# Performance work log

Hardware: AMD Instinct MI355X
Metric: run time of the kernel (lower is better)

## Reference

```python
import jax, jax.numpy as jnp
import numpy as np

N_NODES = 100000


def gcn_conv(x, edge_index, edge_weight, W, b, num_nodes):
    """PyG-style GCNConv: add self-loops, symmetric normalization, aggregate, linear."""
    src, dst = edge_index[0], edge_index[1]
    loop = jnp.arange(num_nodes, dtype=src.dtype)
    src_f = jnp.concatenate([src, loop])
    dst_f = jnp.concatenate([dst, loop])
    w_f = jnp.concatenate([edge_weight, jnp.ones((num_nodes,), dtype=edge_weight.dtype)])

    # symmetric normalization D^-1/2 A_hat D^-1/2
    deg = jax.ops.segment_sum(w_f, dst_f, num_segments=num_nodes)
    dinv = jnp.where(deg > 0, jax.lax.rsqrt(deg), 0.0)
    norm = dinv[src_f] * w_f * dinv[dst_f]  # [E + N]

    h = x @ W  # transform first (small out dim) -> cheaper gather/scatter
    msg = h[src_f] * norm[:, None]  # [E + N, out]
    out = jax.ops.segment_sum(msg, dst_f, num_segments=num_nodes)
    return out + b


def setup_inputs() -> dict:
    key = jax.random.key(0)
    k = jax.random.split(key, 7)
    N, E, F, H, C = N_NODES, 3200000, 64, 32, 5
    x = jax.random.normal(k[0], (N, F), dtype=jnp.float32)
    edge_index = jax.random.randint(k[1], (2, E), 0, N, dtype=jnp.int64)
    edge_attr = jax.random.uniform(k[2], (E,), dtype=jnp.float32)
    # Glorot-style init for GCNConv weights, zero bias (PyG default)
    W1 = jax.random.normal(k[3], (F, H), dtype=jnp.float32) * (1.0 / np.sqrt(F))
    b1 = jnp.zeros((H,), dtype=jnp.float32)
    W2 = jax.random.normal(k[4], (H, C), dtype=jnp.float32) * (1.0 / np.sqrt(H))
    b2 = jnp.zeros((C,), dtype=jnp.float32)
    return {"x": x, "edge_index": edge_index, "edge_attr": edge_attr,
            "W1": W1, "b1": b1, "W2": W2, "b2": b2}


def reference(x, edge_index, edge_attr, W1, b1, W2, b2):
    # Dropout is identity in eval mode.
    x1 = gcn_conv(x, edge_index, edge_attr, W1, b1, N_NODES)
    x1 = jax.nn.relu(x1)
    x2 = gcn_conv(x1, edge_index, edge_attr, W2, b2, N_NODES)
    return (x2, x1)
```

## Files before the change

kernel.cpp:

```cpp
#include <hip/hip_runtime.h>

#define NN 100000
#define NE 3200000
#define FIN 64
#define FH 32
#define FO 5
#define NB 1000
#define NPB 100
#define NBIN (4*NPB)
#define QDIV 25000
#define GC 512
#define EPB (NE/GC)
#define KPT 25
#define APAD 6252
#define DPAD 6272
#define CAP 3584
#define WQS 32767.f
#define WQI (1.0f/32767.f)

__device__ __forceinline__ int detect64(const int* __restrict__ ei, int* sflag, int tid) {
    if (tid < 64) {
        int v = ei[2 * tid + 1];
        unsigned long long m = __ballot(v == 0);
        if (tid == 0) *sflag = (m == ~0ULL) ? 1 : 0;
    }
    __syncthreads();
    return *sflag;
}

__device__ __forceinline__ unsigned bf16r(float f) {
    unsigned u = __float_as_uint(f);
    return (u + 0x7FFFu + ((u >> 16) & 1u)) >> 16;
}
__device__ __forceinline__ float blo(unsigned u) { return __uint_as_float(u << 16); }
__device__ __forceinline__ float bhi(unsigned u) { return __uint_as_float(u & 0xFFFF0000u); }

__global__ void k_fillC(const int* __restrict__ ei, const float* __restrict__ w,
                        int* __restrict__ cntRM, int* __restrict__ locRM,
                        unsigned* __restrict__ edata_a, unsigned char* __restrict__ edata_d) {
    __shared__ unsigned stage_a[EPB];
    __shared__ unsigned char stage_d[EPB];
    __shared__ int hist[NB];
    __shared__ int hoff[NB];
    __shared__ int sscan[256];
    __shared__ int sflag;
    int tid = threadIdx.x, g = blockIdx.x;
    for (int i = tid; i < NB; i += 256) hist[i] = 0;
    int is64 = detect64(ei, &sflag, tid);
    __syncthreads();
    int base = g * EPB;
    int myd[KPT];
#pragma unroll
    for (int k = 0; k < KPT; ++k) {
        int e = base + tid + k * 256;
        int dst = -1;
        if (e < base + EPB) {
            dst = is64 ? ei[2 * NE + 2 * e] : ei[NE + e];
            atomicAdd(&hist[dst / NPB], 1);
        }
        myd[k] = dst;
    }
    __syncthreads();
    for (int i = tid; i < NB; i += 256) cntRM[g * NB + i] = hist[i];
    int b0 = tid * 4;
    int c0 = (b0 + 0 < NB) ? hist[b0 + 0] : 0;
    int c1 = (b0 + 1 < NB) ? hist[b0 + 1] : 0;
    int c2 = (b0 + 2 < NB) ? hist[b0 + 2] : 0;
    int c3 = (b0 + 3 < NB) ? hist[b0 + 3] : 0;
    sscan[tid] = c0 + c1 + c2 + c3;
    __syncthreads();
    for (int off = 1; off < 256; off <<= 1) {
        int v = (tid >= off) ? sscan[tid - off] : 0;
        __syncthreads();
        sscan[tid] += v;
        __syncthreads();
    }
    int excl = sscan[tid] - (c0 + c1 + c2 + c3);
    if (b0 + 0 < NB) { hoff[b0 + 0] = excl;                locRM[g * NB + b0 + 0] = excl; }
    if (b0 + 1 < NB) { hoff[b0 + 1] = excl + c0;           locRM[g * NB + b0 + 1] = excl + c0; }
    if (b0 + 2 < NB) { hoff[b0 + 2] = excl + c0 + c1;      locRM[g * NB + b0 + 2] = excl + c0 + c1; }
    if (b0 + 3 < NB) { hoff[b0 + 3] = excl + c0 + c1 + c2; locRM[g * NB + b0 + 3] = excl + c0 + c1 + c2; }
    __syncthreads();
#pragma unroll
    for (int k = 0; k < KPT; ++k) {
        int e = base + tid + k * 256;
        if (e < base + EPB) {
            int src = is64 ? ei[2 * e] : ei[e];
            int dst = myd[k];
            int b = dst / NPB;
            int dloc = dst - b * NPB;
            unsigned wq = (unsigned)(w[e] * WQS + 0.5f);
            int pos = atomicAdd(&hoff[b], 1);
            stage_a[pos] = (unsigned)src | (wq << 17);
            stage_d[pos] = (unsigned char)dloc;
        }
    }
    __syncthreads();
    unsigned* ga = edata_a + (size_t)g * APAD;
    int4* ga4 = (int4*)ga;
    const int NI4 = EPB / 4;
    for (int i = tid; i < NI4; i += 256) {
        int4 v;
        v.x = (int)stage_a[4 * i];     v.y = (int)stage_a[4 * i + 1];
        v.z = (int)stage_a[4 * i + 2]; v.w = (int)stage_a[4 * i + 3];
        ga4[i] = v;
    }
    if (tid < EPB - NI4 * 4) ga[NI4 * 4 + tid] = stage_a[NI4 * 4 + tid];
    unsigned* gd = (unsigned*)(edata_d + (size_t)g * DPAD);
    const int ND = (EPB + 3) / 4;
    for (int i = tid; i < ND; i += 256) {
        unsigned b0v = stage_d[4 * i];
        unsigned b1v = (4 * i + 1 < EPB) ? stage_d[4 * i + 1] : 0;
        unsigned b2v = (4 * i + 2 < EPB) ? stage_d[4 * i + 2] : 0;
        unsigned b3v = (4 * i + 3 < EPB) ? stage_d[4 * i + 3] : 0;
        gd[i] = b0v | (b1v << 8) | (b2v << 16) | (b3v << 24);
    }
}

__global__ __launch_bounds__(512) void k_nodecsr(
        const int* __restrict__ cntRM, const int* __restrict__ locRM,
        const unsigned* __restrict__ edata_a, const unsigned char* __restrict__ edata_d,
        unsigned* __restrict__ edata2,
        int* __restrict__ rowS, int* __restrict__ rowE, float* __restrict__ dinv) {
    __shared__ unsigned s1a[CAP];
    __shared__ unsigned char s1d[CAP];
    __shared__ unsigned s2a[CAP];
    __shared__ int cnt[NBIN];
    __shared__ int loc[NBIN];
    __shared__ int cur[NBIN];
    __shared__ int sc[512];
    __shared__ int sBlen;
    int bi = blockIdx.x, tid = threadIdx.x;
    int b = (bi & 7) * (NB / 8) + (bi >> 3);
    int base = b * CAP;
    int g = tid;
    int len  = cntRM[g * NB + b];
    int lloc = locRM[g * NB + b];
    const unsigned* A = edata_a + (size_t)g * APAD + lloc;
    const unsigned char* D = edata_d + (size_t)g * DPAD + lloc;
    for (int i = tid; i < NBIN; i += 512) cnt[i] = 0;
    sc[tid] = len;
    __syncthreads();
    for (int off = 1; off < 512; off <<= 1) {
        int x = (tid >= off) ? sc[tid - off] : 0;
        __syncthreads();
        sc[tid] += x;
        __syncthreads();
    }
    int sdst = sc[tid] - len;
    if (tid == 511) sBlen = sc[511];
    __syncthreads();
    int blen = sBlen;
    if (blen <= CAP) {
        for (int k = 0; k < len; ++k) {
            unsigned a = A[k];
            int dloc = D[k];
            int src = (int)(a & 0x1FFFF);
            atomicAdd(&cnt[(dloc << 2) | (src / QDIV)], 1);
            s1a[sdst + k] = a;
            s1d[sdst + k] = (unsigned char)dloc;
        }
        __syncthreads();
        int v = (tid < NBIN) ? cnt[tid] : 0;
        sc[tid] = v;
        __syncthreads();
        for (int off = 1; off < 512; off <<= 1) {
            int x = (tid >= off) ? sc[tid - off] : 0;
            __syncthreads();
            sc[tid] += x;
            __syncthreads();
        }
        if (tid < NBIN) { loc[tid] = sc[tid] - v; cur[tid] = sc[tid] - v; }
        __syncthreads();
        if (tid < NPB) {
            rowS[b * NPB + tid] = base + loc[4 * tid];
            rowE[b * NPB + tid] = base + ((tid == NPB - 1) ? blen : loc[4 * tid + 4]);
        }
        for (int j = tid; j < blen; j += 512) {
            unsigned a = s1a[j];
            int dloc = s1d[j];
            int src = (int)(a & 0x1FFFF);
            int pos = atomicAdd(&cur[(dloc << 2) | (src / QDIV)], 1);
            s2a[pos] = a;
        }
        __syncthreads();
        if (tid < NPB) {
            int e0 = loc[4 * tid];
            int e1 = (tid == NPB - 1) ? blen : loc[4 * tid + 4];
            int isum = 0;
            for (int j = e0; j < e1; ++j) isum += (int)(s2a[j] >> 17);
            dinv[b * NPB + tid] = rsqrtf(1.0f + (float)isum * WQI);
        }
        for (int j = tid; j < blen; j += 512) edata2[base + j] = s2a[j];
    } else {
        int* degI = (int*)s1a;
        if (tid < NPB) degI[tid] = 0;
        __syncthreads();
        for (int k = 0; k < len; ++k) {
            unsigned a = A[k];
            int dloc = D[k];
            int src = (int)(a & 0x1FFFF);
            atomicAdd(&cnt[(dloc << 2) | (src / QDIV)], 1);
            atomicAdd(&degI[dloc], (int)(a >> 17));
        }
        __syncthreads();
        int v = (tid < NBIN) ? cnt[tid] : 0;
        sc[tid] = v;
        __syncthreads();
        for (int off = 1; off < 512; off <<= 1) {
            int x = (tid >= off) ? sc[tid - off] : 0;
            __syncthreads();
            sc[tid] += x;
            __syncthreads();
        }
        if (tid < NBIN) { loc[tid] = sc[tid] - v; cur[tid] = base + sc[tid] - v; }
        __syncthreads();
        if (tid < NPB) {
            int e1 = (tid == NPB - 1) ? blen : loc[4 * tid + 4];
            if (e1 > CAP) e1 = CAP;
            int e0 = loc[4 * tid]; if (e0 > CAP) e0 = CAP;
            rowS[b * NPB + tid] = base + e0;
            rowE[b * NPB + tid] = base + e1;
            dinv[b * NPB + tid] = rsqrtf(1.0f + (float)degI[tid] * WQI);
        }
        __syncthreads();
        for (int k = 0; k < len; ++k) {
            unsigned a = A[k];
            int dloc = D[k];
            int src = (int)(a & 0x1FFFF);
            int pos = atomicAdd(&cur[(dloc << 2) | (src / QDIV)], 1);
            if (pos < base + CAP) edata2[pos] = a;
        }
    }
}

__global__ void k_gemm1(const float* __restrict__ x, const float* __restrict__ W1,
                        const float* __restrict__ dinv, unsigned* __restrict__ hs1b) {
    __shared__ float Ws[FIN * FH];
    __shared__ float Xs[16 * FIN];
    int tid = threadIdx.x;
    for (int i = tid; i < FIN * FH; i += 256) Ws[i] = W1[i];
    int row0 = blockIdx.x * 16;
    for (int i = tid; i < 16 * FIN; i += 256) Xs[i] = x[row0 * FIN + i];
    __syncthreads();
    int l = tid & 15, r = tid >> 4;
    int n = row0 + r;
    float a0 = 0.f, a1 = 0.f;
    const float* xr = &Xs[r * FIN];
#pragma unroll
    for (int f = 0; f < FIN; ++f) {
        float xv = xr[f];
        a0 += xv * Ws[f * FH + 2 * l];
        a1 += xv * Ws[f * FH + 2 * l + 1];
    }
    float di = dinv[n];
    hs1b[n * 16 + l] = bf16r(di * a0) | (bf16r(di * a1) << 16);
}

__global__ void k_pull1(const int* __restrict__ rowS, const int* __restrict__ rowE,
                        const unsigned* __restrict__ ed,
                        const unsigned* __restrict__ hs1b, const float* __restrict__ dinv,
                        const float* __restrict__ b1, const float* __restrict__ W2,
                        float* __restrict__ x1out, unsigned* __restrict__ hs2b) {
    __shared__ float Ws2[FH * FO];
    int tid = threadIdx.x;
    if (tid < FH * FO) Ws2[tid] = W2[tid];
    __syncthreads();
    int l = tid & 15;
    int n = blockIdx.x * 16 + (tid >> 4);
    int s = rowS[n], t = rowE[n];
    unsigned su = hs1b[n * 16 + l];
    float a0 = blo(su), a1 = bhi(su);
    int i = s;
    for (; i + 8 <= t; i += 8) {
        unsigned c0 = ed[i],     c1 = ed[i + 1], c2 = ed[i + 2], c3 = ed[i + 3];
        unsigned c4 = ed[i + 4], c5 = ed[i + 5], c6 = ed[i + 6], c7 = ed[i + 7];
        unsigned u0 = hs1b[(c0 & 0x1FFFF) * 16 + l];
        unsigned u1 = hs1b[(c1 & 0x1FFFF) * 16 + l];
        unsigned u2 = hs1b[(c2 & 0x1FFFF) * 16 + l];
        unsigned u3 = hs1b[(c3 & 0x1FFFF) * 16 + l];
        unsigned u4 = hs1b[(c4 & 0x1FFFF) * 16 + l];
        unsigned u5 = hs1b[(c5 & 0x1FFFF) * 16 + l];
        unsigned u6 = hs1b[(c6 & 0x1FFFF) * 16 + l];
        unsigned u7 = hs1b[(c7 & 0x1FFFF) * 16 + l];
        float w0 = (float)(c0 >> 17) * WQI, w1 = (float)(c1 >> 17) * WQI;
        float w2 = (float)(c2 >> 17) * WQI, w3 = (float)(c3 >> 17) * WQI;
        float w4 = (float)(c4 >> 17) * WQI, w5 = (float)(c5 >> 17) * WQI;
        float w6 = (float)(c6 >> 17) * WQI, w7 = (float)(c7 >> 17) * WQI;
        a0 += w0 * blo(u0); a1 += w0 * bhi(u0);
        a0 += w1 * blo(u1); a1 += w1 * bhi(u1);
        a0 += w2 * blo(u2); a1 += w2 * bhi(u2);
        a0 += w3 * blo(u3); a1 += w3 * bhi(u3);
        a0 += w4 * blo(u4); a1 += w4 * bhi(u4);
        a0 += w5 * blo(u5); a1 += w5 * bhi(u5);
        a0 += w6 * blo(u6); a1 += w6 * bhi(u6);
        a0 += w7 * blo(u7); a1 += w7 * bhi(u7);
    }
    for (; i < t; ++i) {
        unsigned c = ed[i];
        unsigned u = hs1b[(c & 0x1FFFF) * 16 + l];
        float we = (float)(c >> 17) * WQI;
        a0 += we * blo(u); a1 += we * bhi(u);
    }
    float di = dinv[n];
    float v0 = di * a0 + b1[2 * l];
    float v1 = di * a1 + b1[2 * l + 1];
    v0 = (v0 > 0.f) ? v0 : 0.f;
    v1 = (v1 > 0.f) ? v1 : 0.f;
    float2 st; st.x = v0; st.y = v1;
    *(float2*)&x1out[n * FH + 2 * l] = st;
    float hv[6];
    hv[5] = 0.f;
#pragma unroll
    for (int c = 0; c < FO; ++c) {
        float pr = v0 * Ws2[(2 * l) * FO + c] + v1 * Ws2[(2 * l + 1) * FO + c];
        pr += __shfl_xor(pr, 1, 16);
        pr += __shfl_xor(pr, 2, 16);
        pr += __shfl_xor(pr, 4, 16);
        pr += __shfl_xor(pr, 8, 16);
        hv[c] = di * pr;
    }
    if (l < 3) hs2b[n * 4 + l] = bf16r(hv[2 * l]) | (bf16r(hv[2 * l + 1]) << 16);
}

__global__ void k_pull2(const int* __restrict__ rowS, const int* __restrict__ rowE,
                        const unsigned* __restrict__ ed,
                        const unsigned* __restrict__ hs2b, const float* __restrict__ dinv,
                        const float* __restrict__ b2, float* __restrict__ out) {
    int tid = threadIdx.x;
    int c = tid & 7;
    int cm = (c < FO) ? c : 0;
    int wj = cm >> 1, hh = cm & 1;
    int n = blockIdx.x * 32 + (tid >> 3);
    int s = rowS[n], t = rowE[n];
    unsigned us = hs2b[n * 4 + wj];
    float acc = hh ? bhi(us) : blo(us);
    int i = s;
    for (; i + 8 <= t; i += 8) {
        unsigned c0 = ed[i],     c1 = ed[i + 1], c2 = ed[i + 2], c3 = ed[i + 3];
        unsigned c4 = ed[i + 4], c5 = ed[i + 5], c6 = ed[i + 6], c7 = ed[i + 7];
        unsigned u0 = hs2b[(c0 & 0x1FFFF) * 4 + wj];
        unsigned u1 = hs2b[(c1 & 0x1FFFF) * 4 + wj];
        unsigned u2 = hs2b[(c2 & 0x1FFFF) * 4 + wj];
        unsigned u3 = hs2b[(c3 & 0x1FFFF) * 4 + wj];
        unsigned u4 = hs2b[(c4 & 0x1FFFF) * 4 + wj];
        unsigned u5 = hs2b[(c5 & 0x1FFFF) * 4 + wj];
        unsigned u6 = hs2b[(c6 & 0x1FFFF) * 4 + wj];
        unsigned u7 = hs2b[(c7 & 0x1FFFF) * 4 + wj];
        acc += (float)(c0 >> 17) * WQI * (hh ? bhi(u0) : blo(u0));
        acc += (float)(c1 >> 17) * WQI * (hh ? bhi(u1) : blo(u1));
        acc += (float)(c2 >> 17) * WQI * (hh ? bhi(u2) : blo(u2));
        acc += (float)(c3 >> 17) * WQI * (hh ? bhi(u3) : blo(u3));
        acc += (float)(c4 >> 17) * WQI * (hh ? bhi(u4) : blo(u4));
        acc += (float)(c5 >> 17) * WQI * (hh ? bhi(u5) : blo(u5));
        acc += (float)(c6 >> 17) * WQI * (hh ? bhi(u6) : blo(u6));
        acc += (float)(c7 >> 17) * WQI * (hh ? bhi(u7) : blo(u7));
    }
    for (; i < t; ++i) {
        unsigned cc = ed[i];
        unsigned u = hs2b[(cc & 0x1FFFF) * 4 + wj];
        acc += (float)(cc >> 17) * WQI * (hh ? bhi(u) : blo(u));
    }
    if (c < FO) out[n * FO + c] = dinv[n] * acc + b2[c];
}

extern "C" void kernel_launch(void* const* d_in, const int* in_sizes, int n_in,
                              void* d_out, int out_size, void* d_ws, size_t ws_size,
                              hipStream_t stream) {
    const float* x  = (const float*)d_in[0];
    const int*   ei = (const int*)d_in[1];
    const float* w  = (const float*)d_in[2];
    const float* W1 = (const float*)d_in[3];
    const float* b1 = (const float*)d_in[4];
    const float* W2 = (const float*)d_in[5];
    const float* b2 = (const float*)d_in[6];
    float* out = (float*)d_out;
    float* ws  = (float*)d_ws;

    unsigned*      edata_a = (unsigned*)ws;
    unsigned char* edata_d = (unsigned char*)(ws + 3300000);
    unsigned*      edata2  = (unsigned*)(ws + 6400000);
    float*         dinv    = ws + 10000000;
    int*           rowS    = (int*)(ws + 10100000);
    int*           rowE    = (int*)(ws + 10200000);
    int*           cntRM   = (int*)(ws + 12800000);
    int*           locRM   = (int*)(ws + 13312000);
    unsigned*      hs1b    = (unsigned*)ws;
    unsigned*      hs2b    = (unsigned*)(ws + 1600000);

    float* x1 = out + NN * FO;

    k_fillC<<<GC, 256, 0, stream>>>(ei, w, cntRM, locRM, edata_a, edata_d);
    k_nodecsr<<<NB, 512, 0, stream>>>(cntRM, locRM, edata_a, edata_d, edata2, rowS, rowE, dinv);
    k_gemm1<<<NN / 16, 256, 0, stream>>>(x, W1, dinv, hs1b);
    k_pull1<<<NN / 16, 256, 0, stream>>>(rowS, rowE, edata2, hs1b, dinv, b1, W2, x1, hs2b);
    k_pull2<<<NN / 32, 256, 0, stream>>>(rowS, rowE, edata2, hs2b, dinv, b2, out);
}
```

Before: 232.8 us.

## Split layer-1 aggregation into two feature-half passes for cache-resident gathers

The bf16 hidden features are stored as two separate 16-feature halves, and the layer-1 pull kernel runs twice, once per half. Each pass gathers from a 3.2 MB table instead of 6.4 MB, so the random gathers are more likely to hit in cache. The partial layer-2 projection from the first half goes through a temporary buffer and is combined in the second pass. Edge-list loads become nontemporal. The cost is reading the edge list twice plus an extra kernel launch and intermediate traffic.

```diff
diff --git a/kernel.cpp b/kernel.cpp
--- a/kernel.cpp
+++ b/kernel.cpp
@@ -235,7 +235,8 @@
 }
 
 __global__ void k_gemm1(const float* __restrict__ x, const float* __restrict__ W1,
-                        const float* __restrict__ dinv, unsigned* __restrict__ hs1b) {
+                        const float* __restrict__ dinv,
+                        unsigned* __restrict__ hsA, unsigned* __restrict__ hsB) {
     __shared__ float Ws[FIN * FH];
     __shared__ float Xs[16 * FIN];
     int tid = threadIdx.x;
@@ -254,35 +255,45 @@
         a1 += xv * Ws[f * FH + 2 * l + 1];
     }
     float di = dinv[n];
-    hs1b[n * 16 + l] = bf16r(di * a0) | (bf16r(di * a1) << 16);
-}
-
-__global__ void k_pull1(const int* __restrict__ rowS, const int* __restrict__ rowE,
-                        const unsigned* __restrict__ ed,
-                        const unsigned* __restrict__ hs1b, const float* __restrict__ dinv,
-                        const float* __restrict__ b1, const float* __restrict__ W2,
-                        float* __restrict__ x1out, unsigned* __restrict__ hs2b) {
-    __shared__ float Ws2[FH * FO];
+    unsigned pk = bf16r(di * a0) | (bf16r(di * a1) << 16);
+    if (l < 8) hsA[n * 8 + l] = pk;
+    else       hsB[n * 8 + (l - 8)] = pk;
+}
+
+template<int HALF>
+__global__ void k_pull1h(const int* __restrict__ rowS, const int* __restrict__ rowE,
+                         const unsigned* __restrict__ ed,
+                         const unsigned* __restrict__ hs, const float* __restrict__ dinv,
+                         const float* __restrict__ b1, const float* __restrict__ W2,
+                         float* __restrict__ x1out, float* __restrict__ hvpart,
+                         unsigned* __restrict__ hs2b) {
+    __shared__ float Ws2[16 * FO];
     int tid = threadIdx.x;
-    if (tid < FH * FO) Ws2[tid] = W2[tid];
-    __syncthreads();
-    int l = tid & 15;
-    int n = blockIdx.x * 16 + (tid >> 4);
+    if (tid < 16 * FO) Ws2[tid] = W2[HALF * 16 * FO + tid];
+    __syncthreads();
+    int l = tid & 7;
+    int n = blockIdx.x * 32 + (tid >> 3);
     int s = rowS[n], t = rowE[n];
-    unsigned su = hs1b[n * 16 + l];
+    unsigned su = hs[n * 8 + l];
     float a0 = blo(su), a1 = bhi(su);
     int i = s;
     for (; i + 8 <= t; i += 8) {
-        unsigned c0 = ed[i],     c1 = ed[i + 1], c2 = ed[i + 2], c3 = ed[i + 3];
-        unsigned c4 = ed[i + 4], c5 = ed[i + 5], c6 = ed[i + 6], c7 = ed[i + 7];
-        unsigned u0 = hs1b[(c0 & 0x1FFFF) * 16 + l];
-        unsigned u1 = hs1b[(c1 & 0x1FFFF) * 16 + l];
-        unsigned u2 = hs1b[(c2 & 0x1FFFF) * 16 + l];
-        unsigned u3 = hs1b[(c3 & 0x1FFFF) * 16 + l];
-        unsigned u4 = hs1b[(c4 & 0x1FFFF) * 16 + l];
-        unsigned u5 = hs1b[(c5 & 0x1FFFF) * 16 + l];
-        unsigned u6 = hs1b[(c6 & 0x1FFFF) * 16 + l];
-        unsigned u7 = hs1b[(c7 & 0x1FFFF) * 16 + l];
+        unsigned c0 = __builtin_nontemporal_load(ed + i);
+        unsigned c1 = __builtin_nontemporal_load(ed + i + 1);
+        unsigned c2 = __builtin_nontemporal_load(ed + i + 2);
+        unsigned c3 = __builtin_nontemporal_load(ed + i + 3);
+        unsigned c4 = __builtin_nontemporal_load(ed + i + 4);
+        unsigned c5 = __builtin_nontemporal_load(ed + i + 5);
+        unsigned c6 = __builtin_nontemporal_load(ed + i + 6);
+        unsigned c7 = __builtin_nontemporal_load(ed + i + 7);
+        unsigned u0 = hs[(c0 & 0x1FFFF) * 8 + l];
+        unsigned u1 = hs[(c1 & 0x1FFFF) * 8 + l];
+        unsigned u2 = hs[(c2 & 0x1FFFF) * 8 + l];
+        unsigned u3 = hs[(c3 & 0x1FFFF) * 8 + l];
+        unsigned u4 = hs[(c4 & 0x1FFFF) * 8 + l];
+        unsigned u5 = hs[(c5 & 0x1FFFF) * 8 + l];
+        unsigned u6 = hs[(c6 & 0x1FFFF) * 8 + l];
+        unsigned u7 = hs[(c7 & 0x1FFFF) * 8 + l];
         float w0 = (float)(c0 >> 17) * WQI, w1 = (float)(c1 >> 17) * WQI;
         float w2 = (float)(c2 >> 17) * WQI, w3 = (float)(c3 >> 17) * WQI;
         float w4 = (float)(c4 >> 17) * WQI, w5 = (float)(c5 >> 17) * WQI;
@@ -297,30 +308,42 @@
         a0 += w7 * blo(u7); a1 += w7 * bhi(u7);
     }
     for (; i < t; ++i) {
-        unsigned c = ed[i];
-        unsigned u = hs1b[(c & 0x1FFFF) * 16 + l];
+        unsigned c = __builtin_nontemporal_load(ed + i);
+        unsigned u = hs[(c & 0x1FFFF) * 8 + l];
         float we = (float)(c >> 17) * WQI;
         a0 += we * blo(u); a1 += we * bhi(u);
     }
     float di = dinv[n];
-    float v0 = di * a0 + b1[2 * l];
-    float v1 = di * a1 + b1[2 * l + 1];
+    float v0 = di * a0 + b1[HALF * 16 + 2 * l];
+    float v1 = di * a1 + b1[HALF * 16 + 2 * l + 1];
     v0 = (v0 > 0.f) ? v0 : 0.f;
     v1 = (v1 > 0.f) ? v1 : 0.f;
     float2 st; st.x = v0; st.y = v1;
-    *(float2*)&x1out[n * FH + 2 * l] = st;
-    float hv[6];
-    hv[5] = 0.f;
+    *(float2*)&x1out[n * FH + HALF * 16 + 2 * l] = st;
+    float hv[FO];
 #pragma unroll
     for (int c = 0; c < FO; ++c) {
         float pr = v0 * Ws2[(2 * l) * FO + c] + v1 * Ws2[(2 * l + 1) * FO + c];
-        pr += __shfl_xor(pr, 1, 16);
-        pr += __shfl_xor(pr, 2, 16);
-        pr += __shfl_xor(pr, 4, 16);
-        pr += __shfl_xor(pr, 8, 16);
-        hv[c] = di * pr;
-    }
-    if (l < 3) hs2b[n * 4 + l] = bf16r(hv[2 * l]) | (bf16r(hv[2 * l + 1]) << 16);
+        pr += __shfl_xor(pr, 1, 8);
+        pr += __shfl_xor(pr, 2, 8);
+        pr += __shfl_xor(pr, 4, 8);
+        hv[c] = pr;
+    }
+    if (HALF == 0) {
+        float sv = (l == 0) ? hv[0] : (l == 1) ? hv[1] : (l == 2) ? hv[2]
+                 : (l == 3) ? hv[3] : hv[4];
+        if (l < FO) hvpart[n * 5 + l] = sv;
+    } else {
+        if (l < 3) {
+            float e0 = (l == 0) ? hv[0] : (l == 1) ? hv[2] : hv[4];
+            float e1 = (l == 0) ? hv[1] : (l == 1) ? hv[3] : 0.f;
+            float p0 = hvpart[n * 5 + 2 * l];
+            float p1 = (2 * l + 1 < FO) ? hvpart[n * 5 + 2 * l + 1] : 0.f;
+            float t0 = di * (e0 + p0);
+            float t1 = (2 * l + 1 < FO) ? di * (e1 + p1) : 0.f;
+            hs2b[n * 4 + l] = bf16r(t0) | (bf16r(t1) << 16);
+        }
+    }
 }
 
 __global__ void k_pull2(const int* __restrict__ rowS, const int* __restrict__ rowE,
@@ -385,14 +408,17 @@
     int*           rowE    = (int*)(ws + 10200000);
     int*           cntRM   = (int*)(ws + 12800000);
     int*           locRM   = (int*)(ws + 13312000);
-    unsigned*      hs1b    = (unsigned*)ws;
+    unsigned*      hsA     = (unsigned*)ws;
+    unsigned*      hsB     = (unsigned*)(ws + 800000);
     unsigned*      hs2b    = (unsigned*)(ws + 1600000);
+    float*         hvpart  = ws + 2000000;
 
     float* x1 = out + NN * FO;
 
     k_fillC<<<GC, 256, 0, stream>>>(ei, w, cntRM, locRM, edata_a, edata_d);
     k_nodecsr<<<NB, 512, 0, stream>>>(cntRM, locRM, edata_a, edata_d, edata2, rowS, rowE, dinv);
-    k_gemm1<<<NN / 16, 256, 0, stream>>>(x, W1, dinv, hs1b);
-    k_pull1<<<NN / 16, 256, 0, stream>>>(rowS, rowE, edata2, hs1b, dinv, b1, W2, x1, hs2b);
+    k_gemm1<<<NN / 16, 256, 0, stream>>>(x, W1, dinv, hsA, hsB);
+    k_pull1h<0><<<NN / 32, 256, 0, stream>>>(rowS, rowE, edata2, hsA, dinv, b1, W2, x1, hvpart, hs2b);
+    k_pull1h<1><<<NN / 32, 256, 0, stream>>>(rowS, rowE, edata2, hsB, dinv, b1, W2, x1, hvpart, hs2b);
     k_pull2<<<NN / 32, 256, 0, stream>>>(rowS, rowE, edata2, hs2b, dinv, b2, out);
 }
```

Result: slower. 273.0 us (+17.3%).
